# Performance work log

Hardware: AMD Instinct MI355X
Metric: run time of the kernel (lower is better)

Reference implementation:

```python
import jax, jax.numpy as jnp
import numpy as np

N_NODES = 50000
N_EDGES = 800000
IN_FEATS = 128
HID = 64
HEADS = 3
NUM_CLASSES = 8
ATTN_SLOPE = 0.2   # DGL GATConv leaky_relu slope on attention logits
ACT_SLOPE = 0.01   # nn.LeakyReLU default


def setup_inputs() -> dict:
    key = jax.random.key(0)
    ks = jax.random.split(key, 40)
    inp = {}
    inp["x"] = jax.random.normal(ks[0], (N_NODES, IN_FEATS), dtype=jnp.float32)
    inp["src"] = jax.random.randint(ks[1], (N_EDGES,), 0, N_NODES)
    inp["dst"] = jax.random.randint(ks[2], (N_EDGES,), 0, N_NODES)
    dims_in = [IN_FEATS, HID, HID, HID, HID]
    i = 3
    for l, din in enumerate(dims_in, start=1):
        inp[f"W{l}"] = jax.random.normal(ks[i], (din, HEADS * HID), dtype=jnp.float32) / np.float32(np.sqrt(din)); i += 1
        inp[f"b{l}"] = jnp.zeros((HEADS * HID,), dtype=jnp.float32)
        inp[f"al{l}"] = jax.random.normal(ks[i], (HEADS, HID), dtype=jnp.float32) * 0.1; i += 1
        inp[f"ar{l}"] = jax.random.normal(ks[i], (HEADS, HID), dtype=jnp.float32) * 0.1; i += 1
    inp["Wo"] = jax.random.normal(ks[i], (HID, NUM_CLASSES), dtype=jnp.float32) / np.float32(np.sqrt(HID)); i += 1
    inp["bo"] = jnp.zeros((NUM_CLASSES,), dtype=jnp.float32)
    return inp


def _gatconv(h, W, b, al, ar, src, dst):
    # h: [N, din] -> feat: [N, H, F]
    feat = (h @ W).reshape(N_NODES, HEADS, HID)
    el = jnp.einsum('nhf,hf->nh', feat, al)   # [N, H]
    er = jnp.einsum('nhf,hf->nh', feat, ar)   # [N, H]
    e = jax.nn.leaky_relu(el[src] + er[dst], ATTN_SLOPE)        # [E, H]
    # numerically-stable edge softmax segmented by destination node
    m = jax.ops.segment_max(e, dst, num_segments=N_NODES)      # [N, H]
    ex = jnp.exp(e - m[dst])                                   # [E, H]
    denom = jax.ops.segment_sum(ex, dst, num_segments=N_NODES)  # [N, H]
    alpha = ex / denom[dst]                                    # [E, H]
    msg = alpha[:, :, None] * feat[src]                        # [E, H, F]
    out = jax.ops.segment_sum(msg, dst, num_segments=N_NODES)  # [N, H, F]
    return out + b.reshape(HEADS, HID)


def reference(x, src, dst,
              W1, b1, al1, ar1,
              W2, b2, al2, ar2,
              W3, b3, al3, ar3,
              W4, b4, al4, ar4,
              W5, b5, al5, ar5,
              Wo, bo):
    layers = [(W1, b1, al1, ar1), (W2, b2, al2, ar2), (W3, b3, al3, ar3),
              (W4, b4, al4, ar4), (W5, b5, al5, ar5)]
    h = x
    for (W, b, al, ar) in layers:
        h = jax.nn.leaky_relu(_gatconv(h, W, b, al, ar, src, dst), ACT_SLOPE)
        h = h.mean(axis=1)  # mean over heads -> [N, F]
    return h @ Wo + bo      # [N, num_classes]
```

## Files before the change

### kernel.cpp

```cpp
#include <hip/hip_runtime.h>
#include <hip/hip_fp16.h>
#include <cstdint>

#define N_NODES 50000
#define N_EDGES 800000
#define IN_FEATS 128
#define HID 64
#define HEADS 3
#define NUM_CLASSES 8
#define ATTN_SLOPE 0.2f
#define ACT_SLOPE 0.01f

#define NGRP 8
#define GRP_NODES 6250
#define NCHUNK 128
#define CHUNK 6250

typedef _Float16 half8 __attribute__((ext_vector_type(8)));
typedef float f32x4 __attribute__((ext_vector_type(4)));

__device__ __forceinline__ float lrelu(float x, float s) { return x > 0.f ? x : s * x; }

__global__ __launch_bounds__(256) void k_deg(const int* __restrict__ dst, int* __restrict__ deg, int E) {
    int grp = blockIdx.x & (NGRP - 1);
    int chunk = blockIdx.x >> 3;
    int lo = grp * GRP_NODES, hi = lo + GRP_NODES;
    int s = chunk * CHUNK, e = min(E, s + CHUNK);
    for (int i = s + (int)threadIdx.x; i < e; i += 256) {
        int d = dst[i];
        if (d >= lo && d < hi) atomicAdd(&deg[d], 1);
    }
}

__global__ __launch_bounds__(256) void k_scan1(const int* __restrict__ deg, int* __restrict__ off,
                                               int* __restrict__ bsum, int n) {
    __shared__ int wtot[4];
    int tid = threadIdx.x;
    int lane = tid & 63, wid = tid >> 6;
    int base = blockIdx.x * 2048 + tid * 8;
    int v[8];
    if (base + 8 <= n) {
        int4 a = *(const int4*)&deg[base];
        int4 b = *(const int4*)&deg[base + 4];
        v[0] = a.x; v[1] = a.y; v[2] = a.z; v[3] = a.w;
        v[4] = b.x; v[5] = b.y; v[6] = b.z; v[7] = b.w;
    } else {
#pragma unroll
        for (int j = 0; j < 8; ++j) v[j] = (base + j < n) ? deg[base + j] : 0;
    }
    int s[8];
    s[0] = v[0];
#pragma unroll
    for (int j = 1; j < 8; ++j) s[j] = s[j - 1] + v[j];
    int t = s[7];
    int incl = t;
    for (int o = 1; o < 64; o <<= 1) {
        int u = __shfl_up(incl, o);
        if (lane >= o) incl += u;
    }
    int excl = incl - t;
    if (lane == 63) wtot[wid] = incl;
    __syncthreads();
    int wprefix = 0;
    for (int w = 0; w < wid; ++w) wprefix += wtot[w];
    int base_off = wprefix + excl;
#pragma unroll
    for (int j = 0; j < 8; ++j)
        if (base + j < n) off[base + j] = base_off + s[j] - v[j];
    if (tid == 0) bsum[blockIdx.x] = wtot[0] + wtot[1] + wtot[2] + wtot[3];
}

__global__ __launch_bounds__(64) void k_scan2(int* __restrict__ bsum, int nb) {
    int tid = threadIdx.x;
    int v = (tid < nb) ? bsum[tid] : 0;
    int incl = v;
    for (int o = 1; o < 64; o <<= 1) {
        int u = __shfl_up(incl, o);
        if (tid >= o) incl += u;
    }
    if (tid < nb) bsum[tid] = incl - v;
}

__global__ __launch_bounds__(256) void k_scan3(int* __restrict__ off, const int* __restrict__ bsum,
                                               int n, int E) {
    int i = blockIdx.x * blockDim.x + threadIdx.x;
    if (i < n) off[i] += bsum[i >> 11];
    if (i == 0) off[n] = E;
}

__global__ __launch_bounds__(256) void k_fill(const int* __restrict__ src, const int* __restrict__ dst,
                                              const int* __restrict__ off, int* __restrict__ cur,
                                              int* __restrict__ ssrc, int E) {
    int grp = blockIdx.x & (NGRP - 1);
    int chunk = blockIdx.x >> 3;
    int lo = grp * GRP_NODES, hi = lo + GRP_NODES;
    int s = chunk * CHUNK, e = min(E, s + CHUNK);
    for (int i = s + (int)threadIdx.x; i < e; i += 256) {
        int d = dst[i];
        if (d >= lo && d < hi) {
            int p = atomicAdd(&cur[d], 1);
            ssrc[off[d] + p] = src[i];
        }
    }
}

__global__ __launch_bounds__(256) void k_xcast(const float* __restrict__ x, _Float16* __restrict__ xh, int n8) {
    int i = blockIdx.x * blockDim.x + threadIdx.x;
    if (i < n8) {
        float4 a = *(const float4*)&x[i * 8];
        float4 b = *(const float4*)&x[i * 8 + 4];
        _Float16 v[8] = {(_Float16)a.x, (_Float16)a.y, (_Float16)a.z, (_Float16)a.w,
                         (_Float16)b.x, (_Float16)b.y, (_Float16)b.z, (_Float16)b.w};
        *(uint4*)&xh[i * 8] = *(uint4*)v;
    }
}

__global__ __launch_bounds__(256) void k_wcast(const float* __restrict__ W1, const float* __restrict__ W2,
                                               const float* __restrict__ W3, const float* __restrict__ W4,
                                               const float* __restrict__ W5, _Float16* __restrict__ Wt) {
    int i = blockIdx.x * blockDim.x + threadIdx.x;
    if (i >= 24576 + 4 * 12288) return;
    const float* W; int din; int idx; _Float16* out;
    if (i < 24576) { W = W1; din = 128; idx = i; out = Wt; }
    else {
        int j = i - 24576; int l = j / 12288; idx = j % 12288;
        W = (l == 0) ? W2 : (l == 1) ? W3 : (l == 2) ? W4 : W5;
        din = 64;
        out = Wt + 24576 + l * 12288;
    }
    int col = idx / din, k = idx % din;
    out[idx] = (_Float16)W[k * 192 + col];
}

__global__ __launch_bounds__(64) void k_gemm(const _Float16* __restrict__ h, const _Float16* __restrict__ Wt,
                                             const float* __restrict__ al, const float* __restrict__ ar,
                                             _Float16* __restrict__ feat,
                                             float* __restrict__ el, float* __restrict__ er,
                                             int N, int din) {
    int bid = blockIdx.x;
    int head = bid % 3;
    int rt0 = bid / 3;
    int row0 = rt0 * 32;
    int c0 = head * 64;
    int lane = threadIdx.x;
    int l15 = lane & 15;
    int koff = (lane >> 4) * 8;

    f32x4 acc[2][4] = {};
    int r0 = min(row0 + l15, N - 1);
    int r1 = min(row0 + 16 + l15, N - 1);
    const _Float16* wbase = Wt + (size_t)(c0 + l15) * din + koff;
    const _Float16* hbase0 = h + (size_t)r0 * din + koff;
    const _Float16* hbase1 = h + (size_t)r1 * din + koff;

    int nkb = din >> 5;
    for (int kb = 0; kb < nkb; ++kb) {
        int kb32 = kb * 32;
        half8 b0 = *(const half8*)&wbase[kb32];
        half8 b1 = *(const half8*)&wbase[16 * din + kb32];
        half8 b2 = *(const half8*)&wbase[32 * din + kb32];
        half8 b3 = *(const half8*)&wbase[48 * din + kb32];
        half8 a0 = *(const half8*)&hbase0[kb32];
        half8 a1 = *(const half8*)&hbase1[kb32];
        acc[0][0] = __builtin_amdgcn_mfma_f32_16x16x32_f16(a0, b0, acc[0][0], 0, 0, 0);
        acc[0][1] = __builtin_amdgcn_mfma_f32_16x16x32_f16(a0, b1, acc[0][1], 0, 0, 0);
        acc[0][2] = __builtin_amdgcn_mfma_f32_16x16x32_f16(a0, b2, acc[0][2], 0, 0, 0);
        acc[0][3] = __builtin_amdgcn_mfma_f32_16x16x32_f16(a0, b3, acc[0][3], 0, 0, 0);
        acc[1][0] = __builtin_amdgcn_mfma_f32_16x16x32_f16(a1, b0, acc[1][0], 0, 0, 0);
        acc[1][1] = __builtin_amdgcn_mfma_f32_16x16x32_f16(a1, b1, acc[1][1], 0, 0, 0);
        acc[1][2] = __builtin_amdgcn_mfma_f32_16x16x32_f16(a1, b2, acc[1][2], 0, 0, 0);
        acc[1][3] = __builtin_amdgcn_mfma_f32_16x16x32_f16(a1, b3, acc[1][3], 0, 0, 0);
    }

    float alv[4], arv[4];
#pragma unroll
    for (int ct = 0; ct < 4; ++ct) {
        alv[ct] = al[c0 + ct * 16 + l15];
        arv[ct] = ar[c0 + ct * 16 + l15];
    }

#pragma unroll
    for (int rt = 0; rt < 2; ++rt) {
#pragma unroll
        for (int r = 0; r < 4; ++r) {
            int row = row0 + rt * 16 + (lane >> 4) * 4 + r;
            bool ok = (row < N);
            float c0v = acc[rt][0][r], c1v = acc[rt][1][r], c2v = acc[rt][2][r], c3v = acc[rt][3][r];
            if (ok) {
                size_t base = (size_t)row * 192 + c0;
                feat[base + l15]      = (_Float16)c0v;
                feat[base + 16 + l15] = (_Float16)c1v;
                feat[base + 32 + l15] = (_Float16)c2v;
                feat[base + 48 + l15] = (_Float16)c3v;
            }
            float pl = c0v * alv[0] + c1v * alv[1] + c2v * alv[2] + c3v * alv[3];
            float pr = c0v * arv[0] + c1v * arv[1] + c2v * arv[2] + c3v * arv[3];
            for (int o = 1; o < 16; o <<= 1) {
                pl += __shfl_xor(pl, o);
                pr += __shfl_xor(pr, o);
            }
            if (ok && l15 == 0) {
                el[row * HEADS + head] = pl;
                er[row * HEADS + head] = pr;
            }
        }
    }
}

__global__ __launch_bounds__(64) void k_agg(const int* __restrict__ off, const int* __restrict__ ssrc,
                                            const float* __restrict__ el, const float* __restrict__ er,
                                            const __half* __restrict__ feat, const float* __restrict__ b,
                                            __half* __restrict__ hout, int N) {
    __shared__ float4 ebuf[64];
    int wid = blockIdx.x;
    int lane = threadIdx.x;
    if (wid >= N) return;
    int start = off[wid], end = off[wid + 1];
    int cnt = end - start;
    float er0 = er[wid * HEADS + 0];
    float er1 = er[wid * HEADS + 1];
    float er2 = er[wid * HEADS + 2];
    float acc0 = 0.f, acc1 = 0.f, acc2 = 0.f;
    float den0 = 0.f, den1 = 0.f, den2 = 0.f;

    if (cnt <= 64) {
        int s0 = 0;
        float ea = -3.4e38f, eb = -3.4e38f, ec = -3.4e38f;
        if (lane < cnt) {
            s0 = ssrc[start + lane];
            ea = lrelu(el[s0 * HEADS + 0] + er0, ATTN_SLOPE);
            eb = lrelu(el[s0 * HEADS + 1] + er1, ATTN_SLOPE);
            ec = lrelu(el[s0 * HEADS + 2] + er2, ATTN_SLOPE);
        }
        float ma = ea, mb = eb, mc = ec;
        for (int o = 32; o > 0; o >>= 1) {
            ma = fmaxf(ma, __shfl_xor(ma, o));
            mb = fmaxf(mb, __shfl_xor(mb, o));
            mc = fmaxf(mc, __shfl_xor(mc, o));
        }
        float xa = (lane < cnt) ? __expf(ea - ma) : 0.f;
        float xb = (lane < cnt) ? __expf(eb - mb) : 0.f;
        float xc = (lane < cnt) ? __expf(ec - mc) : 0.f;
        float da = xa, db = xb, dc = xc;
        for (int o = 32; o > 0; o >>= 1) {
            da += __shfl_xor(da, o);
            db += __shfl_xor(db, o);
            dc += __shfl_xor(dc, o);
        }
        den0 = da; den1 = db; den2 = dc;
        ebuf[lane] = make_float4(__int_as_float(s0), xa, xb, xc);
        int t = 0;
        for (; t + 4 <= cnt; t += 4) {
            float4 v0 = ebuf[t + 0];
            float4 v1 = ebuf[t + 1];
            float4 v2 = ebuf[t + 2];
            float4 v3 = ebuf[t + 3];
            const __half* f0 = feat + (size_t)__float_as_int(v0.x) * 192 + lane;
            const __half* f1 = feat + (size_t)__float_as_int(v1.x) * 192 + lane;
            const __half* f2 = feat + (size_t)__float_as_int(v2.x) * 192 + lane;
            const __half* f3 = feat + (size_t)__float_as_int(v3.x) * 192 + lane;
            float p00 = __half2float(f0[0]), p01 = __half2float(f0[64]), p02 = __half2float(f0[128]);
            float p10 = __half2float(f1[0]), p11 = __half2float(f1[64]), p12 = __half2float(f1[128]);
            float p20 = __half2float(f2[0]), p21 = __half2float(f2[64]), p22 = __half2float(f2[128]);
            float p30 = __half2float(f3[0]), p31 = __half2float(f3[64]), p32 = __half2float(f3[128]);
            acc0 += v0.y * p00; acc1 += v0.z * p01; acc2 += v0.w * p02;
            acc0 += v1.y * p10; acc1 += v1.z * p11; acc2 += v1.w * p12;
            acc0 += v2.y * p20; acc1 += v2.z * p21; acc2 += v2.w * p22;
            acc0 += v3.y * p30; acc1 += v3.z * p31; acc2 += v3.w * p32;
        }
        for (; t < cnt; ++t) {
            float4 v = ebuf[t];
            const __half* fr = feat + (size_t)__float_as_int(v.x) * 192 + lane;
            acc0 += v.y * __half2float(fr[0]);
            acc1 += v.z * __half2float(fr[64]);
            acc2 += v.w * __half2float(fr[128]);
        }
    } else {
        float ma = -3.4e38f, mb = -3.4e38f, mc = -3.4e38f;
        for (int j = start + lane; j < end; j += 64) {
            int s = ssrc[j];
            ma = fmaxf(ma, lrelu(el[s * HEADS + 0] + er0, ATTN_SLOPE));
            mb = fmaxf(mb, lrelu(el[s * HEADS + 1] + er1, ATTN_SLOPE));
            mc = fmaxf(mc, lrelu(el[s * HEADS + 2] + er2, ATTN_SLOPE));
        }
        for (int o = 32; o > 0; o >>= 1) {
            ma = fmaxf(ma, __shfl_xor(ma, o));
            mb = fmaxf(mb, __shfl_xor(mb, o));
            mc = fmaxf(mc, __shfl_xor(mc, o));
        }
        float da = 0.f, db = 0.f, dc = 0.f;
        for (int j0 = start; j0 < end; j0 += 64) {
            int jj = j0 + lane;
            int s0 = 0;
            float xa = 0.f, xb = 0.f, xc = 0.f;
            if (jj < end) {
                s0 = ssrc[jj];
                xa = __expf(lrelu(el[s0 * HEADS + 0] + er0, ATTN_SLOPE) - ma);
                xb = __expf(lrelu(el[s0 * HEADS + 1] + er1, ATTN_SLOPE) - mb);
                xc = __expf(lrelu(el[s0 * HEADS + 2] + er2, ATTN_SLOPE) - mc);
            }
            da += xa; db += xb; dc += xc;
            ebuf[lane] = make_float4(__int_as_float(s0), xa, xb, xc);
            int c = min(64, end - j0);
            int t = 0;
            for (; t + 4 <= c; t += 4) {
                float4 v0 = ebuf[t + 0];
                float4 v1 = ebuf[t + 1];
                float4 v2 = ebuf[t + 2];
                float4 v3 = ebuf[t + 3];
                const __half* f0 = feat + (size_t)__float_as_int(v0.x) * 192 + lane;
                const __half* f1 = feat + (size_t)__float_as_int(v1.x) * 192 + lane;
                const __half* f2 = feat + (size_t)__float_as_int(v2.x) * 192 + lane;
                const __half* f3 = feat + (size_t)__float_as_int(v3.x) * 192 + lane;
                float p00 = __half2float(f0[0]), p01 = __half2float(f0[64]), p02 = __half2float(f0[128]);
                float p10 = __half2float(f1[0]), p11 = __half2float(f1[64]), p12 = __half2float(f1[128]);
                float p20 = __half2float(f2[0]), p21 = __half2float(f2[64]), p22 = __half2float(f2[128]);
                float p30 = __half2float(f3[0]), p31 = __half2float(f3[64]), p32 = __half2float(f3[128]);
                acc0 += v0.y * p00; acc1 += v0.z * p01; acc2 += v0.w * p02;
                acc0 += v1.y * p10; acc1 += v1.z * p11; acc2 += v1.w * p12;
                acc0 += v2.y * p20; acc1 += v2.z * p21; acc2 += v2.w * p22;
                acc0 += v3.y * p30; acc1 += v3.z * p31; acc2 += v3.w * p32;
            }
            for (; t < c; ++t) {
                float4 v = ebuf[t];
                const __half* fr = feat + (size_t)__float_as_int(v.x) * 192 + lane;
                acc0 += v.y * __half2float(fr[0]);
                acc1 += v.z * __half2float(fr[64]);
                acc2 += v.w * __half2float(fr[128]);
            }
        }
        for (int o = 32; o > 0; o >>= 1) {
            da += __shfl_xor(da, o);
            db += __shfl_xor(db, o);
            dc += __shfl_xor(dc, o);
        }
        den0 = da; den1 = db; den2 = dc;
    }

    float v0 = (cnt > 0) ? acc0 / den0 : 0.f;
    float v1 = (cnt > 0) ? acc1 / den1 : 0.f;
    float v2 = (cnt > 0) ? acc2 / den2 : 0.f;
    float hsum = lrelu(v0 + b[lane], ACT_SLOPE)
               + lrelu(v1 + b[64 + lane], ACT_SLOPE)
               + lrelu(v2 + b[128 + lane], ACT_SLOPE);
    hout[wid * 64 + lane] = __float2half(hsum * (1.f / 3.f));
}

__global__ __launch_bounds__(256) void k_out(const __half* __restrict__ h, const float* __restrict__ Wo,
                                             const float* __restrict__ bo, float* __restrict__ out, int N) {
    __shared__ float Hl[32][65];
    __shared__ float Wl[64 * 8];
    int tid = threadIdx.x;
    int n0 = blockIdx.x * 32;
    for (int i = tid; i < 32 * 64; i += 256) {
        int r = i >> 6, k = i & 63;
        Hl[r][k] = (n0 + r < N) ? __half2float(h[(n0 + r) * 64 + k]) : 0.f;
    }
    for (int i = tid; i < 512; i += 256) Wl[i] = Wo[i];
    __syncthreads();
    int r = tid >> 3, c = tid & 7;
    float acc = 0.f;
    for (int k = 0; k < 64; ++k) acc += Hl[r][k] * Wl[k * 8 + c];
    int row = n0 + r;
    if (row < N) out[row * 8 + c] = acc + bo[c];
}

extern "C" void kernel_launch(void* const* d_in, const int* in_sizes, int n_in,
                              void* d_out, int out_size, void* d_ws, size_t ws_size,
                              hipStream_t stream) {
    const float* x  = (const float*)d_in[0];
    const int* src  = (const int*)d_in[1];
    const int* dst  = (const int*)d_in[2];
    const float *W[5], *b[5], *al[5], *ar[5];
    for (int l = 0; l < 5; ++l) {
        W[l]  = (const float*)d_in[3 + l * 4];
        b[l]  = (const float*)d_in[4 + l * 4];
        al[l] = (const float*)d_in[5 + l * 4];
        ar[l] = (const float*)d_in[6 + l * 4];
    }
    const float* Wo = (const float*)d_in[23];
    const float* bo = (const float*)d_in[24];
    float* out = (float*)d_out;

    char* ws = (char*)d_ws;
    auto alloc = [&](size_t bytes) {
        char* p = ws;
        ws += (bytes + 255) & ~size_t(255);
        return p;
    };
    _Float16* feat = (_Float16*)alloc(sizeof(_Float16) * (size_t)N_NODES * 192);
    float* el      = (float*)alloc(sizeof(float) * (size_t)N_NODES * HEADS);
    float* er      = (float*)alloc(sizeof(float) * (size_t)N_NODES * HEADS);
    _Float16* xh   = (_Float16*)alloc(sizeof(_Float16) * (size_t)N_NODES * IN_FEATS);
    _Float16* h0   = (_Float16*)alloc(sizeof(_Float16) * (size_t)N_NODES * 64);
    _Float16* h1   = (_Float16*)alloc(sizeof(_Float16) * (size_t)N_NODES * 64);
    _Float16* wt   = (_Float16*)alloc(sizeof(_Float16) * (24576 + 4 * 12288));
    int* deg    = (int*)alloc(sizeof(int) * N_NODES);
    int* off    = (int*)alloc(sizeof(int) * (N_NODES + 1));
    int* cur    = (int*)alloc(sizeof(int) * N_NODES);
    int* ssrc   = (int*)alloc(sizeof(int) * N_EDGES);
    int* bsum   = (int*)alloc(sizeof(int) * 64);

    const int NB = (N_NODES + 2047) / 2048;
    (void)hipMemsetAsync(deg, 0, sizeof(int) * N_NODES, stream);
    (void)hipMemsetAsync(cur, 0, sizeof(int) * N_NODES, stream);
    k_deg<<<NCHUNK * NGRP, 256, 0, stream>>>(dst, deg, N_EDGES);
    k_scan1<<<NB, 256, 0, stream>>>(deg, off, bsum, N_NODES);
    k_scan2<<<1, 64, 0, stream>>>(bsum, NB);
    k_scan3<<<(N_NODES + 255) / 256, 256, 0, stream>>>(off, bsum, N_NODES, N_EDGES);
    k_fill<<<NCHUNK * NGRP, 256, 0, stream>>>(src, dst, off, cur, ssrc, N_EDGES);
    k_xcast<<<(N_NODES * IN_FEATS / 8 + 255) / 256, 256, 0, stream>>>(x, xh, N_NODES * IN_FEATS / 8);
    k_wcast<<<(24576 + 4 * 12288 + 255) / 256, 256, 0, stream>>>(W[0], W[1], W[2], W[3], W[4], wt);

    const _Float16* hin = xh;
    _Float16* hbuf[2] = {h0, h1};
    const _Float16* wts[5] = {wt, wt + 24576, wt + 24576 + 12288, wt + 24576 + 2 * 12288, wt + 24576 + 3 * 12288};
    int din = IN_FEATS;
    for (int l = 0; l < 5; ++l) {
        int nrt = (N_NODES + 31) / 32;
        k_gemm<<<nrt * 3, 64, 0, stream>>>(hin, wts[l], al[l], ar[l], feat, el, er, N_NODES, din);
        _Float16* hn = hbuf[l & 1];
        k_agg<<<N_NODES, 64, 0, stream>>>(off, ssrc, el, er,
                                          (const __half*)feat, b[l],
                                          (__half*)hn, N_NODES);
        hin = hn;
        din = HID;
    }
    k_out<<<(N_NODES + 31) / 32, 256, 0, stream>>>((const __half*)hin, Wo, bo, out, N_NODES);
}
```

Baseline: 514.4 us.

## Fold attention vectors into weights and compute el/er via extra MFMA

Precomputes W·al and W·ar per head as extra fp16 weight columns so the GEMM produces el/er directly through one additional MFMA per row tile, removing the epilogue dot products and shuffle reductions. The feat store is changed to a packed 4-half write per lane with a permuted column layout, and the aggregation kernel reads through a matching permuted index. This trades some precision (fp16 attention projections) and extra tiny setup kernels for a lighter GEMM epilogue and wider stores.

Result: slower. 684.5 us (+33.1%).

```diff
diff --git a/kernel.cpp b/kernel.cpp
--- a/kernel.cpp
+++ b/kernel.cpp
@@ -132,24 +132,41 @@
     out[idx] = (_Float16)W[k * 192 + col];
 }
 
+__global__ __launch_bounds__(384) void k_acast(const float* __restrict__ W, const float* __restrict__ al,
+                                               const float* __restrict__ ar, _Float16* __restrict__ alx,
+                                               int din) {
+    int tid = blockIdx.x * blockDim.x + threadIdx.x;
+    if (tid >= 3 * din) return;
+    int hh = tid / din, k = tid % din;
+    float sl = 0.f, sr = 0.f;
+    for (int f = 0; f < 64; ++f) {
+        float w = W[(size_t)k * 192 + hh * 64 + f];
+        sl += w * al[hh * 64 + f];
+        sr += w * ar[hh * 64 + f];
+    }
+    alx[(size_t)(hh * 16 + 0) * din + k] = (_Float16)sl;
+    alx[(size_t)(hh * 16 + 1) * din + k] = (_Float16)sr;
+}
+
 __global__ __launch_bounds__(64) void k_gemm(const _Float16* __restrict__ h, const _Float16* __restrict__ Wt,
-                                             const float* __restrict__ al, const float* __restrict__ ar,
+                                             const _Float16* __restrict__ alx,
                                              _Float16* __restrict__ feat,
                                              float* __restrict__ el, float* __restrict__ er,
                                              int N, int din) {
     int bid = blockIdx.x;
     int head = bid % 3;
-    int rt0 = bid / 3;
-    int row0 = rt0 * 32;
+    int row0 = (bid / 3) * 32;
     int c0 = head * 64;
     int lane = threadIdx.x;
     int l15 = lane & 15;
     int koff = (lane >> 4) * 8;
 
     f32x4 acc[2][4] = {};
+    f32x4 acce[2] = {};
     int r0 = min(row0 + l15, N - 1);
     int r1 = min(row0 + 16 + l15, N - 1);
     const _Float16* wbase = Wt + (size_t)(c0 + l15) * din + koff;
+    const _Float16* xbase = alx + (size_t)(head * 16 + l15) * din + koff;
     const _Float16* hbase0 = h + (size_t)r0 * din + koff;
     const _Float16* hbase1 = h + (size_t)r1 * din + koff;
 
@@ -160,23 +177,19 @@
         half8 b1 = *(const half8*)&wbase[16 * din + kb32];
         half8 b2 = *(const half8*)&wbase[32 * din + kb32];
         half8 b3 = *(const half8*)&wbase[48 * din + kb32];
+        half8 bx = *(const half8*)&xbase[kb32];
         half8 a0 = *(const half8*)&hbase0[kb32];
         half8 a1 = *(const half8*)&hbase1[kb32];
         acc[0][0] = __builtin_amdgcn_mfma_f32_16x16x32_f16(a0, b0, acc[0][0], 0, 0, 0);
         acc[0][1] = __builtin_amdgcn_mfma_f32_16x16x32_f16(a0, b1, acc[0][1], 0, 0, 0);
         acc[0][2] = __builtin_amdgcn_mfma_f32_16x16x32_f16(a0, b2, acc[0][2], 0, 0, 0);
         acc[0][3] = __builtin_amdgcn_mfma_f32_16x16x32_f16(a0, b3, acc[0][3], 0, 0, 0);
+        acce[0]   = __builtin_amdgcn_mfma_f32_16x16x32_f16(a0, bx, acce[0], 0, 0, 0);
         acc[1][0] = __builtin_amdgcn_mfma_f32_16x16x32_f16(a1, b0, acc[1][0], 0, 0, 0);
         acc[1][1] = __builtin_amdgcn_mfma_f32_16x16x32_f16(a1, b1, acc[1][1], 0, 0, 0);
         acc[1][2] = __builtin_amdgcn_mfma_f32_16x16x32_f16(a1, b2, acc[1][2], 0, 0, 0);
         acc[1][3] = __builtin_amdgcn_mfma_f32_16x16x32_f16(a1, b3, acc[1][3], 0, 0, 0);
-    }
-
-    float alv[4], arv[4];
-#pragma unroll
-    for (int ct = 0; ct < 4; ++ct) {
-        alv[ct] = al[c0 + ct * 16 + l15];
-        arv[ct] = ar[c0 + ct * 16 + l15];
+        acce[1]   = __builtin_amdgcn_mfma_f32_16x16x32_f16(a1, bx, acce[1], 0, 0, 0);
     }
 
 #pragma unroll
@@ -184,24 +197,12 @@
 #pragma unroll
         for (int r = 0; r < 4; ++r) {
             int row = row0 + rt * 16 + (lane >> 4) * 4 + r;
-            bool ok = (row < N);
-            float c0v = acc[rt][0][r], c1v = acc[rt][1][r], c2v = acc[rt][2][r], c3v = acc[rt][3][r];
-            if (ok) {
-                size_t base = (size_t)row * 192 + c0;
-                feat[base + l15]      = (_Float16)c0v;
-                feat[base + 16 + l15] = (_Float16)c1v;
-                feat[base + 32 + l15] = (_Float16)c2v;
-                feat[base + 48 + l15] = (_Float16)c3v;
-            }
-            float pl = c0v * alv[0] + c1v * alv[1] + c2v * alv[2] + c3v * alv[3];
-            float pr = c0v * arv[0] + c1v * arv[1] + c2v * arv[2] + c3v * arv[3];
-            for (int o = 1; o < 16; o <<= 1) {
-                pl += __shfl_xor(pl, o);
-                pr += __shfl_xor(pr, o);
-            }
-            if (ok && l15 == 0) {
-                el[row * HEADS + head] = pl;
-                er[row * HEADS + head] = pr;
+            if (row < N) {
+                _Float16 p[4] = {(_Float16)acc[rt][0][r], (_Float16)acc[rt][1][r],
+                                 (_Float16)acc[rt][2][r], (_Float16)acc[rt][3][r]};
+                *(uint2*)&feat[(size_t)row * 192 + c0 + l15 * 4] = *(uint2*)p;
+                if (l15 == 0) el[row * HEADS + head] = acce[rt][r];
+                else if (l15 == 1) er[row * HEADS + head] = acce[rt][r];
             }
         }
     }
@@ -215,6 +216,7 @@
     int wid = blockIdx.x;
     int lane = threadIdx.x;
     if (wid >= N) return;
+    int po = ((lane & 15) << 2) + (lane >> 4);
     int start = off[wid], end = off[wid + 1];
     int cnt = end - start;
     float er0 = er[wid * HEADS + 0];
@@ -255,10 +257,10 @@
             float4 v1 = ebuf[t + 1];
             float4 v2 = ebuf[t + 2];
             float4 v3 = ebuf[t + 3];
-            const __half* f0 = feat + (size_t)__float_as_int(v0.x) * 192 + lane;
-            const __half* f1 = feat + (size_t)__float_as_int(v1.x) * 192 + lane;
-            const __half* f2 = feat + (size_t)__float_as_int(v2.x) * 192 + lane;
-            const __half* f3 = feat + (size_t)__float_as_int(v3.x) * 192 + lane;
+            const __half* f0 = feat + (size_t)__float_as_int(v0.x) * 192 + po;
+            const __half* f1 = feat + (size_t)__float_as_int(v1.x) * 192 + po;
+            const __half* f2 = feat + (size_t)__float_as_int(v2.x) * 192 + po;
+            const __half* f3 = feat + (size_t)__float_as_int(v3.x) * 192 + po;
             float p00 = __half2float(f0[0]), p01 = __half2float(f0[64]), p02 = __half2float(f0[128]);
             float p10 = __half2float(f1[0]), p11 = __half2float(f1[64]), p12 = __half2float(f1[128]);
             float p20 = __half2float(f2[0]), p21 = __half2float(f2[64]), p22 = __half2float(f2[128]);
@@ -270,7 +272,7 @@
         }
         for (; t < cnt; ++t) {
             float4 v = ebuf[t];
-            const __half* fr = feat + (size_t)__float_as_int(v.x) * 192 + lane;
+            const __half* fr = feat + (size_t)__float_as_int(v.x) * 192 + po;
             acc0 += v.y * __half2float(fr[0]);
             acc1 += v.z * __half2float(fr[64]);
             acc2 += v.w * __half2float(fr[128]);
@@ -308,10 +310,10 @@
                 float4 v1 = ebuf[t + 1];
                 float4 v2 = ebuf[t + 2];
                 float4 v3 = ebuf[t + 3];
-                const __half* f0 = feat + (size_t)__float_as_int(v0.x) * 192 + lane;
-                const __half* f1 = feat + (size_t)__float_as_int(v1.x) * 192 + lane;
-                const __half* f2 = feat + (size_t)__float_as_int(v2.x) * 192 + lane;
-                const __half* f3 = feat + (size_t)__float_as_int(v3.x) * 192 + lane;
+                const __half* f0 = feat + (size_t)__float_as_int(v0.x) * 192 + po;
+                const __half* f1 = feat + (size_t)__float_as_int(v1.x) * 192 + po;
+                const __half* f2 = feat + (size_t)__float_as_int(v2.x) * 192 + po;
+                const __half* f3 = feat + (size_t)__float_as_int(v3.x) * 192 + po;
                 float p00 = __half2float(f0[0]), p01 = __half2float(f0[64]), p02 = __half2float(f0[128]);
                 float p10 = __half2float(f1[0]), p11 = __half2float(f1[64]), p12 = __half2float(f1[128]);
                 float p20 = __half2float(f2[0]), p21 = __half2float(f2[64]), p22 = __half2float(f2[128]);
@@ -323,7 +325,7 @@
             }
             for (; t < c; ++t) {
                 float4 v = ebuf[t];
-                const __half* fr = feat + (size_t)__float_as_int(v.x) * 192 + lane;
+                const __half* fr = feat + (size_t)__float_as_int(v.x) * 192 + po;
                 acc0 += v.y * __half2float(fr[0]);
                 acc1 += v.z * __half2float(fr[64]);
                 acc2 += v.w * __half2float(fr[128]);
@@ -395,6 +397,7 @@
     _Float16* h0   = (_Float16*)alloc(sizeof(_Float16) * (size_t)N_NODES * 64);
     _Float16* h1   = (_Float16*)alloc(sizeof(_Float16) * (size_t)N_NODES * 64);
     _Float16* wt   = (_Float16*)alloc(sizeof(_Float16) * (24576 + 4 * 12288));
+    _Float16* alx  = (_Float16*)alloc(sizeof(_Float16) * (3 * 16 * 128 + 4 * 3 * 16 * 64));
     int* deg    = (int*)alloc(sizeof(int) * N_NODES);
     int* off    = (int*)alloc(sizeof(int) * (N_NODES + 1));
     int* cur    = (int*)alloc(sizeof(int) * N_NODES);
@@ -404,6 +407,7 @@
     const int NB = (N_NODES + 2047) / 2048;
     (void)hipMemsetAsync(deg, 0, sizeof(int) * N_NODES, stream);
     (void)hipMemsetAsync(cur, 0, sizeof(int) * N_NODES, stream);
+    (void)hipMemsetAsync(alx, 0, sizeof(_Float16) * (3 * 16 * 128 + 4 * 3 * 16 * 64), stream);
     k_deg<<<NCHUNK * NGRP, 256, 0, stream>>>(dst, deg, N_EDGES);
     k_scan1<<<NB, 256, 0, stream>>>(deg, off, bsum, N_NODES);
     k_scan2<<<1, 64, 0, stream>>>(bsum, NB);
@@ -412,13 +416,21 @@
     k_xcast<<<(N_NODES * IN_FEATS / 8 + 255) / 256, 256, 0, stream>>>(x, xh, N_NODES * IN_FEATS / 8);
     k_wcast<<<(24576 + 4 * 12288 + 255) / 256, 256, 0, stream>>>(W[0], W[1], W[2], W[3], W[4], wt);
 
+    _Float16* alxs[5];
+    alxs[0] = alx;
+    for (int l = 1; l < 5; ++l) alxs[l] = alx + 3 * 16 * 128 + (l - 1) * 3 * 16 * 64;
+    for (int l = 0; l < 5; ++l) {
+        int din_l = (l == 0) ? IN_FEATS : HID;
+        k_acast<<<1, 384, 0, stream>>>(W[l], al[l], ar[l], alxs[l], din_l);
+    }
+
     const _Float16* hin = xh;
     _Float16* hbuf[2] = {h0, h1};
     const _Float16* wts[5] = {wt, wt + 24576, wt + 24576 + 12288, wt + 24576 + 2 * 12288, wt + 24576 + 3 * 12288};
     int din = IN_FEATS;
     for (int l = 0; l < 5; ++l) {
         int nrt = (N_NODES + 31) / 32;
-        k_gemm<<<nrt * 3, 64, 0, stream>>>(hin, wts[l], al[l], ar[l], feat, el, er, N_NODES, din);
+        k_gemm<<<nrt * 3, 64, 0, stream>>>(hin, wts[l], alxs[l], feat, el, er, N_NODES, din);
         _Float16* hn = hbuf[l & 1];
         k_agg<<<N_NODES, 64, 0, stream>>>(off, ssrc, el, er,
                                           (const __half*)feat, b[l],
```
